# Kernel tuning notes

Hardware: AMD Instinct MI355X
Metric: run time of the kernel (lower is better)

## Reference

```python
import jax, jax.numpy as jnp
import numpy as np

R_MAX = 10.0
NUM_BESSEL = 8
POLY_P = 5
EMB = 64
MLP_DIM = 256
NUM_LAYERS = 3
IN_DIM = 10
OUT_DIM = 1
N_NODES = 256
N_EDGES = 1024
N_GRAPHS = 16
# gated TP output: 0e channel carries 64 scalars + 128 gates (one per gated 1o/2e irrep)
GATE_MUL = {0: 3 * EMB, 1: EMB, 2: EMB}
L0_PATHS = [(0, 0, 0), (0, 1, 1), (0, 2, 2)]  # in_irreps = 64x0e
LN_PATHS = [(0, 0, 0), (1, 1, 0), (2, 2, 0), (0, 1, 1), (1, 0, 1), (1, 2, 1), (2, 1, 1), (0, 2, 2), (2, 0, 2), (1, 1, 2), (2, 2, 2)]

def _npaths(paths):
    d = {0: 0, 1: 0, 2: 0}
    for _, _, l3 in paths:
        d[l3] += 1
    return d

L0_NP = _npaths(L0_PATHS)
LN_NP = _npaths(LN_PATHS)
L0_NUMEL = sum(EMB * GATE_MUL[l3] for _, _, l3 in L0_PATHS)   # 20480
LN_NUMEL = sum(EMB * GATE_MUL[l3] for _, _, l3 in LN_PATHS)   # 69632

# ---- real spherical harmonics, component normalization (||Y_l||^2 = 2l+1) ----
def _sh_np(v):
    x, y, z = v[:, 0], v[:, 1], v[:, 2]
    s15 = np.sqrt(15.0)
    return {0: np.ones((v.shape[0], 1)),
            1: np.sqrt(3.0) * np.stack([x, y, z], 1),
            2: np.stack([s15 * x * y, s15 * y * z, 0.5 * np.sqrt(5.0) * (3 * z * z - 1), s15 * x * z, 0.5 * s15 * (x * x - y * y)], 1)}

def _rot(axis, t):
    c, s = np.cos(t), np.sin(t)
    R = np.eye(3)
    i, j = [(1, 2), (2, 0), (0, 1)][axis]
    R[i, i] = c; R[j, j] = c; R[i, j] = -s; R[j, i] = s
    return R

_PTS = np.random.RandomState(0).randn(64, 3)
_PTS /= np.linalg.norm(_PTS, axis=1, keepdims=True)

def _D(l, R):
    # rep matrix D with Y(Rv) = D @ Y(v), fit by least squares over sample points
    A = _sh_np(_PTS)[l]
    B = _sh_np(_PTS @ R.T)[l]
    return np.linalg.lstsq(A, B, rcond=None)[0].T

def _gen(l, axis, eps=1e-4):
    return (_D(l, _rot(axis, eps)) - _D(l, _rot(axis, -eps))) / (2 * eps)

def _cg(l1, l2, l3):
    # Clebsch-Gordan tensor as null space of the infinitesimal equivariance constraint
    d1, d2, d3 = 2 * l1 + 1, 2 * l2 + 1, 2 * l3 + 1
    rows = []
    for a in range(3):
        J1, J2, J3 = _gen(l1, a), _gen(l2, a), _gen(l3, a)
        rows.append(np.kron(J1.T, np.eye(d2 * d3)) + np.kron(np.eye(d1), np.kron(J2.T, np.eye(d3))) - np.kron(np.eye(d1 * d2), J3))
    _, _, Vh = np.linalg.svd(np.vstack(rows))
    c = Vh[-1].reshape(d1, d2, d3)
    c = c / np.linalg.norm(c)
    c = c * np.sign(c.flat[int(np.argmax(np.abs(c)))])
    return c

CG = {p: jnp.asarray(_cg(*p), jnp.float32) for p in set(LN_PATHS)}

def _sh_jax(u):
    x, y, z = u[..., 0], u[..., 1], u[..., 2]
    s15 = 15.0 ** 0.5
    return {0: jnp.ones_like(x)[:, None],
            1: (3.0 ** 0.5) * jnp.stack([x, y, z], -1),
            2: jnp.stack([s15 * x * y, s15 * y * z, 0.5 * (5.0 ** 0.5) * (3 * z * z - 1), s15 * x * z, 0.5 * s15 * (x * x - y * y)], -1)}

def _radial(r):
    # Bessel radial basis * polynomial cutoff envelope (MACE-style RadialEmbeddingBlock)
    n = jnp.arange(1, NUM_BESSEL + 1, dtype=r.dtype)
    bessel = (2.0 / R_MAX) ** 0.5 * jnp.sin(n * jnp.pi * r[:, None] / R_MAX) / r[:, None]
    x = r / R_MAX
    p = POLY_P
    env = 1.0 - 0.5 * (p + 1) * (p + 2) * x ** p + p * (p + 2) * x ** (p + 1) - 0.5 * p * (p + 1) * x ** (p + 2)
    env = env * (x < 1.0)
    return bessel * env[:, None]

def _conv(h, sh, ef, recv, send, paths, n_per, w1, b1, w2, b2):
    # TensorProductConvLayer: MLP(edge_feats) -> TP weights, CG tensor product, scatter-sum, gate
    E = ef.shape[0]
    w = jax.nn.relu(ef @ w1 + b1) @ w2 + b2  # (E, weight_numel)
    msgs = {0: 0.0, 1: 0.0, 2: 0.0}
    off = 0
    for (l1, l2, l3) in paths:
        mv = GATE_MUL[l3]
        wp = w[:, off:off + EMB * mv].reshape(E, EMB, mv)
        off += EMB * mv
        tmp = jnp.einsum('eui,ej,ijk->euk', h[l1][send], sh[l2], CG[(l1, l2, l3)])
        alpha = float(1.0 / np.sqrt(EMB * n_per[l3]))  # fan-in path normalization
        msgs[l3] = msgs[l3] + alpha * jnp.einsum('euk,euv->evk', tmp, wp)
    agg = {l: jax.ops.segment_sum(msgs[l], recv, num_segments=N_NODES) for l in msgs}
    s = agg[0][..., 0]  # (N, 192): 64 scalars + 128 gates
    return {0: jax.nn.silu(s[:, :EMB])[:, :, None],
            1: agg[1] * jax.nn.sigmoid(s[:, EMB:2 * EMB])[:, :, None],
            2: agg[2] * jax.nn.sigmoid(s[:, 2 * EMB:])[:, :, None]}

def _forward(atoms, pos, edge_index, batch, emb, l0_fc1_w, l0_fc1_b, l0_fc2_w, l0_fc2_b, fcs1_w, fcs1_b, fcs2_w, fcs2_b, pred_w1, pred_b1, pred_w2, pred_b2):
    recv, send = edge_index[0], edge_index[1]
    vec = pos[recv] - pos[send]
    r = jnp.maximum(jnp.linalg.norm(vec, axis=-1), 1e-6)
    sh = _sh_jax(vec / r[:, None])
    ef = _radial(r)
    h = {0: emb[atoms][:, :, None]}  # (N, 64, 1) scalar features
    h_new = _conv(h, sh, ef, recv, send, L0_PATHS, L0_NP, l0_fc1_w, l0_fc1_b, l0_fc2_w, l0_fc2_b)
    h_new[0] = h_new[0] + h[0]  # residual; F.pad means only scalar block overlaps
    h = h_new
    for i in range(NUM_LAYERS - 1):
        h_new = _conv(h, sh, ef, recv, send, LN_PATHS, LN_NP, fcs1_w[i], fcs1_b[i], fcs2_w[i], fcs2_b[i])
        h = {l: h_new[l] + h[l] for l in h_new}
    pooled = jax.ops.segment_sum(h[0][..., 0], batch, num_segments=N_GRAPHS)  # out[:, :emb_dim]
    return jax.nn.relu(pooled @ pred_w1 + pred_b1) @ pred_w2 + pred_b2

def setup_inputs():
    key = jax.random.key(0)
    ks = jax.random.split(key, 12)
    def lin(k, fi, fo):
        return jax.random.normal(k, (fi, fo), jnp.float32) * float(1.0 / np.sqrt(fi))
    return dict(
        atoms=jax.random.randint(ks[0], (N_NODES,), 0, IN_DIM),
        pos=jax.random.normal(ks[1], (N_NODES, 3), jnp.float32) * 2.0,
        edge_index=jax.random.randint(ks[2], (2, N_EDGES), 0, N_NODES),
        batch=jnp.sort(jax.random.randint(ks[3], (N_NODES,), 0, N_GRAPHS)),
        emb=jax.random.normal(ks[4], (IN_DIM, EMB), jnp.float32),
        l0_fc1_w=lin(ks[5], NUM_BESSEL, MLP_DIM), l0_fc1_b=jnp.zeros((MLP_DIM,), jnp.float32),
        l0_fc2_w=lin(ks[6], MLP_DIM, L0_NUMEL), l0_fc2_b=jnp.zeros((L0_NUMEL,), jnp.float32),
        fcs1_w=jax.random.normal(ks[7], (NUM_LAYERS - 1, NUM_BESSEL, MLP_DIM), jnp.float32) * float(1.0 / np.sqrt(NUM_BESSEL)),
        fcs1_b=jnp.zeros((NUM_LAYERS - 1, MLP_DIM), jnp.float32),
        fcs2_w=jax.random.normal(ks[8], (NUM_LAYERS - 1, MLP_DIM, LN_NUMEL), jnp.float32) * float(1.0 / np.sqrt(MLP_DIM)),
        fcs2_b=jnp.zeros((NUM_LAYERS - 1, LN_NUMEL), jnp.float32),
        pred_w1=lin(ks[9], EMB, EMB), pred_b1=jnp.zeros((EMB,), jnp.float32),
        pred_w2=lin(ks[10], EMB, OUT_DIM), pred_b2=jnp.zeros((OUT_DIM,), jnp.float32),
    )

def reference(atoms, pos, edge_index, batch, emb, l0_fc1_w, l0_fc1_b, l0_fc2_w, l0_fc2_b, fcs1_w, fcs1_b, fcs2_w, fcs2_b, pred_w1, pred_b1, pred_w2, pred_b2):
    return _forward(atoms, pos, edge_index, batch, emb, l0_fc1_w, l0_fc1_b, l0_fc2_w, l0_fc2_b, fcs1_w, fcs1_b, fcs2_w, fcs2_b, pred_w1, pred_b1, pred_w2, pred_b2)
```

## Files before the change

### kernel.cpp

```cpp
#include <hip/hip_runtime.h>
#include <hip/hip_bf16.h>
#include <math.h>

#define NE 1024
#define NN 256
#define NG 16
#define EMB 64
#define KD 256
#define BK 64
#define NUMEL_L0 20480
#define NUMEL_LN 69632
#define MSGW 704
#define MAXE 256

typedef __attribute__((ext_vector_type(8))) __bf16 bf16x8;
typedef __attribute__((ext_vector_type(4))) float f32x4;
typedef __attribute__((ext_vector_type(4))) unsigned int u32x4;

__device__ __align__(16) float g_sh[NE * 8];
__device__ __align__(16) float g_ef[NE * 8];
__device__ __align__(16) unsigned short g_hidb[3][NE * KD];
__device__ __align__(16) unsigned short g_w2t0[(size_t)NUMEL_L0 * KD];
__device__ __align__(16) unsigned short g_w2t1[(size_t)NUMEL_LN * KD];
__device__ __align__(16) unsigned short g_w2t2[(size_t)NUMEL_LN * KD];
__device__ __align__(16) unsigned short g_wb[(size_t)NE * NUMEL_LN];
__device__ __align__(16) float g_msgs[NE * MSGW];
__device__ __align__(16) float g_h0[NN * EMB];
__device__ __align__(16) float g_h1[NN * EMB * 3];
__device__ __align__(16) float g_h2[NN * EMB * 5];
__device__ int g_elist[NN * MAXE];
__device__ int g_ecnt[NN];
__device__ float g_cg[363];

__device__ __forceinline__ unsigned short f2b(float x) {
    __hip_bfloat16 h = __float2bfloat16(x);
    return *(unsigned short*)&h;
}
__device__ __forceinline__ float b2f(unsigned short u) {
    __hip_bfloat16 h;
    *(unsigned short*)&h = u;
    return __bfloat162float(h);
}

__device__ __forceinline__ void gld16(const void* g, void* l) {
    __builtin_amdgcn_global_load_lds(
        (const __attribute__((address_space(1))) unsigned int*)g,
        (__attribute__((address_space(3))) unsigned int*)l, 16, 0, 0);
}

struct Path { int l1, l2, d1, d2, d3, mv, off, cgoff, tmpoff; };

__constant__ Path PLN[11] = {
    {0, 0, 1, 1, 1, 192, 0,     0,   0},
    {1, 1, 3, 3, 1, 192, 12288, 1,   64},
    {2, 2, 5, 5, 1, 192, 24576, 10,  128},
    {0, 1, 1, 3, 3, 64,  36864, 35,  192},
    {1, 0, 3, 1, 3, 64,  40960, 44,  384},
    {1, 2, 3, 5, 3, 64,  45056, 53,  576},
    {2, 1, 5, 3, 3, 64,  49152, 98,  768},
    {0, 2, 1, 5, 5, 64,  53248, 143, 960},
    {2, 0, 5, 1, 5, 64,  57344, 168, 1280},
    {1, 1, 3, 3, 5, 64,  61440, 193, 1600},
    {2, 2, 5, 5, 5, 64,  65536, 238, 1920},
};
__constant__ Path PL0[3] = {
    {0, 0, 1, 1, 1, 192, 0,     0,   0},
    {0, 1, 1, 3, 3, 64,  12288, 35,  64},
    {0, 2, 1, 5, 5, 64,  16384, 143, 256},
};

__device__ void init_cg_body() {
    for (int i = 0; i < 363; i++) g_cg[i] = 0.f;
    const float K3 = 0.57735026918962576f;
    const float K5 = 0.44721359549995794f;
    const float A  = 0.31622776601683794f;
    const float B  = 0.18257418583505536f;
    const float C2 = 0.36514837167011072f;
    const float P  = 0.23904572186687872f;
    const float Q  = 0.20701966780270626f;
    const float S  = 0.11952286093343936f;
    g_cg[0] = 1.f;
    for (int i = 0; i < 3; i++) g_cg[1 + i * 3 + i] = K3;
    for (int i = 0; i < 5; i++) g_cg[10 + i * 5 + i] = K5;
    for (int i = 0; i < 3; i++) g_cg[35 + i * 3 + i] = K3;
    for (int i = 0; i < 3; i++) g_cg[44 + i * 3 + i] = K3;
    g_cg[53 + 1]  = A;  g_cg[53 + 15] = A;  g_cg[53 + 20] = A;
    g_cg[53 + 34] = A;  g_cg[53 + 11] = A;  g_cg[53 + 39] = A;
    g_cg[53 + 6]  = -B; g_cg[53 + 22] = -B; g_cg[53 + 38] = C2;
    g_cg[53 + 12] = A;  g_cg[53 + 28] = -A;
    g_cg[98 + 1]  = A;  g_cg[98 + 3]  = A;  g_cg[98 + 14] = A;
    g_cg[98 + 16] = A;  g_cg[98 + 29] = A;  g_cg[98 + 33] = A;
    g_cg[98 + 18] = -B; g_cg[98 + 22] = -B; g_cg[98 + 26] = C2;
    g_cg[98 + 36] = A;  g_cg[98 + 40] = -A;
    for (int i = 0; i < 5; i++) g_cg[143 + i * 5 + i] = K5;
    for (int i = 0; i < 5; i++) g_cg[168 + i * 5 + i] = K5;
    g_cg[193 + 5]  = A;  g_cg[193 + 15] = A;  g_cg[193 + 26] = A;
    g_cg[193 + 36] = A;  g_cg[193 + 13] = A;  g_cg[193 + 33] = A;
    g_cg[193 + 2]  = -B; g_cg[193 + 22] = -B; g_cg[193 + 42] = C2;
    g_cg[193 + 4]  = A;  g_cg[193 + 24] = -A;
    g_cg[238 + 2]   = P;  g_cg[238 + 10]  = P;  g_cg[238 + 50]  = P;
    g_cg[238 + 8]   = -Q; g_cg[238 + 16]  = -Q; g_cg[238 + 28]  = -Q;
    g_cg[238 + 40]  = -Q; g_cg[238 + 76]  = -Q; g_cg[238 + 80]  = -Q;
    g_cg[238 + 32]  = -S; g_cg[238 + 36]  = -S; g_cg[238 + 56]  = -S;
    g_cg[238 + 34]  = Q;  g_cg[238 + 46]  = Q;  g_cg[238 + 106] = Q;
    g_cg[238 + 62]  = -P;
    g_cg[238 + 74]  = P;  g_cg[238 + 114] = P;  g_cg[238 + 122] = P;
    g_cg[238 + 68]  = -S; g_cg[238 + 88]  = -S; g_cg[238 + 92]  = -S;
    g_cg[238 + 94]  = -Q; g_cg[238 + 98]  = -Q; g_cg[238 + 118] = -Q;
}

__global__ __launch_bounds__(256) void k_setup(const int* ei, const float* pos,
                                               const int* atoms, const float* emb,
                                               const float* l0w2, const float* f2w) {
    int bid = blockIdx.x, tid = threadIdx.x;
    if (bid == 0) {
        if (tid == 0) init_cg_body();
        return;
    }
    if (bid <= 4) {
        int e = (bid - 1) * 256 + tid;
        int recv = ei[e], send = ei[NE + e];
        float vx = pos[recv * 3 + 0] - pos[send * 3 + 0];
        float vy = pos[recv * 3 + 1] - pos[send * 3 + 1];
        float vz = pos[recv * 3 + 2] - pos[send * 3 + 2];
        float rn = sqrtf(vx * vx + vy * vy + vz * vz);
        float r = fmaxf(rn, 1e-6f);
        float x = vx / r, y = vy / r, z = vz / r;
        const float S3 = 1.7320508075688772f;
        const float S15 = 3.8729833462074170f;
        const float S5H = 1.1180339887498949f;
        const float S15H = 1.9364916731037085f;
        g_sh[e * 8 + 0] = S3 * x;
        g_sh[e * 8 + 1] = S3 * y;
        g_sh[e * 8 + 2] = S3 * z;
        g_sh[e * 8 + 3] = S15 * x * y;
        g_sh[e * 8 + 4] = S15 * y * z;
        g_sh[e * 8 + 5] = S5H * (3.f * z * z - 1.f);
        g_sh[e * 8 + 6] = S15 * x * z;
        g_sh[e * 8 + 7] = S15H * (x * x - y * y);
        float xr = r * 0.1f;
        float env = 0.f;
        if (xr < 1.f) {
            float x5 = xr * xr * xr * xr * xr;
            env = 1.f - 21.f * x5 + 35.f * x5 * xr - 15.f * x5 * xr * xr;
        }
        const float SB = 0.44721359549995794f;
        const float PI = 3.14159265358979323846f;
        for (int nb = 1; nb <= 8; nb++) {
            g_ef[e * 8 + nb - 1] = SB * sinf((float)nb * PI * r * 0.1f) / r * env;
        }
        return;
    }
    if (bid <= 68) {
        int idx = (bid - 5) * 256 + tid;
        int n = idx / EMB, u = idx % EMB;
        g_h0[idx] = emb[atoms[n] * EMB + u];
        for (int k = 0; k < 3; k++) g_h1[idx * 3 + k] = 0.f;
        for (int k = 0; k < 5; k++) g_h2[idx * 5 + k] = 0.f;
        return;
    }
    if (bid <= 324) {
        int n = bid - 69;
        int lane = tid & 63, w = tid >> 6;
        __shared__ int wsum[4];
        int mask = 0;
#pragma unroll
        for (int i = 0; i < 4; i++) {
            if (ei[tid * 4 + i] == n) mask |= 1 << i;
        }
        int nm = __popc(mask);
        int incl = nm;
#pragma unroll
        for (int off = 1; off < 64; off <<= 1) {
            int v = __shfl_up(incl, off);
            if (lane >= off) incl += v;
        }
        if (lane == 63) wsum[w] = incl;
        __syncthreads();
        int wbase = 0;
        for (int i = 0; i < w; i++) wbase += wsum[i];
        int base = wbase + incl - nm;
#pragma unroll
        for (int i = 0; i < 4; i++) {
            if (mask & (1 << i)) g_elist[n * MAXE + base++] = tid * 4 + i;
        }
        if (tid == 255) g_ecnt[n] = wbase + incl;
        return;
    }
    {
        __shared__ float t[32][33];
        int wbid = bid - 325;
        int lbid, numel;
        const float* w2;
        unsigned short* dst;
        if (wbid < 5120)       { lbid = wbid;         numel = NUMEL_L0; w2 = l0w2; dst = g_w2t0; }
        else if (wbid < 22528) { lbid = wbid - 5120;  numel = NUMEL_LN; w2 = f2w;  dst = g_w2t1; }
        else                   { lbid = wbid - 22528; numel = NUMEL_LN;
                                 w2 = f2w + (size_t)KD * NUMEL_LN; dst = g_w2t2; }
        int n0 = (lbid >> 3) * 32, k0 = (lbid & 7) * 32;
        int tx = tid & 31, ty = tid >> 5;
#pragma unroll
        for (int i = 0; i < 4; i++) {
            int kl = ty * 4 + i;
            t[kl][tx] = w2[(size_t)(k0 + kl) * numel + n0 + tx];
        }
        __syncthreads();
#pragma unroll
        for (int i = 0; i < 4; i++) {
            int nl = ty * 4 + i;
            dst[(size_t)(n0 + nl) * KD + k0 + tx] = f2b(t[tx][nl]);
        }
    }
}

__global__ __launch_bounds__(256) void k_hid_all(const float* l0w1, const float* l0b1,
                                                 const float* f1w, const float* f1b) {
    int r = blockIdx.x;
    int layer = r >> 10, e = r & 1023;
    const float* w1 = layer == 0 ? l0w1 : f1w + (size_t)(layer - 1) * 8 * KD;
    const float* b1 = layer == 0 ? l0b1 : f1b + (size_t)(layer - 1) * KD;
    int m = threadIdx.x;
    float acc = b1[m];
    for (int nb = 0; nb < 8; nb++) acc += g_ef[e * 8 + nb] * w1[nb * KD + m];
    g_hidb[layer][e * KD + m] = f2b(fmaxf(acc, 0.f));
}

__global__ __launch_bounds__(256) void k_gemm_mfma(const float* b2, int numel, int layer) {
    __shared__ unsigned short S[16384];
    int tid = threadIdx.x;
    int lane = tid & 63, wid = tid >> 6;
    int wm = wid >> 1, wn = wid & 1;
    int id = blockIdx.x;
    int xcd = id & 7;
    int q = id >> 3;
    int mb = q & 7;
    int ytile = q >> 3;
    int nt = xcd + 8 * ytile;
    int m0 = mb * 128, n0 = nt * 128;
    int fr = lane & 15;
    int ko = (lane >> 4) * 8;

    const unsigned short* w2t = layer == 0 ? g_w2t0 : (layer == 1 ? g_w2t1 : g_w2t2);
    const char* gA = (const char*)g_hidb[layer];
    const char* gB = (const char*)w2t;
    f32x4 acc[4][4] = {};

    for (int kst = 0; kst < 4; kst++) {
#pragma unroll
        for (int i = 0; i < 4; i++) {
            int L = wid * 4096 + i * 1024 + lane * 16;
            int row = L >> 7, p = L & 127;
            int sp = p ^ ((row & 7) << 4);
            gld16(gA + ((size_t)(m0 + row) * KD + kst * BK) * 2 + sp, (char*)S + L);
        }
#pragma unroll
        for (int i = 0; i < 4; i++) {
            int L = wid * 4096 + i * 1024 + lane * 16;
            int row = L >> 7, p = L & 127;
            int sp = p ^ ((row & 7) << 4);
            gld16(gB + ((size_t)(n0 + row) * KD + kst * BK) * 2 + sp, (char*)S + 16384 + L);
        }
        __syncthreads();
#pragma unroll
        for (int ks = 0; ks < 2; ks++) {
            int klb = ks * 64 + ko * 2;
            bf16x8 af[4], bf_[4];
#pragma unroll
            for (int f = 0; f < 4; f++) {
                int ra = wm * 64 + f * 16 + fr;
                af[f] = *(bf16x8*)((char*)S + ra * 128 + (klb ^ ((ra & 7) << 4)));
                int rb = wn * 64 + f * 16 + fr;
                bf_[f] = *(bf16x8*)((char*)S + 16384 + rb * 128 + (klb ^ ((rb & 7) << 4)));
            }
#pragma unroll
            for (int i = 0; i < 4; i++)
#pragma unroll
                for (int j = 0; j < 4; j++)
                    acc[i][j] = __builtin_amdgcn_mfma_f32_16x16x32_bf16(af[i], bf_[j], acc[i][j], 0, 0, 0);
        }
        __syncthreads();
    }

#pragma unroll
    for (int j = 0; j < 4; j++) {
        int colL = wn * 64 + j * 16 + fr;
        float bb = b2[n0 + colL];
#pragma unroll
        for (int i = 0; i < 4; i++) {
#pragma unroll
            for (int r = 0; r < 4; r++) {
                int rowL = wm * 64 + i * 16 + (lane >> 4) * 4 + r;
                *(unsigned short*)((char*)S + rowL * 256 + ((colL * 2) ^ ((rowL & 7) << 4))) =
                    f2b(acc[i][j][r] + bb);
            }
        }
    }
    __syncthreads();
    for (int c = tid; c < 2048; c += 256) {
        int row = c >> 4, p16 = (c & 15) * 16;
        u32x4 v = *(u32x4*)((char*)S + row * 256 + (p16 ^ ((row & 7) << 4)));
        *(u32x4*)((char*)(g_wb + (size_t)(m0 + row) * numel + n0) + p16) = v;
    }
}

__global__ __launch_bounds__(256) void k_contract(const int* ei, int layer) {
    int e = blockIdx.x;
    int grp = blockIdx.y;
    int tid = threadIdx.x;
    __shared__ float tmp[1280];
    int layer0 = (layer == 0) ? 1 : 0;
    int numel = layer0 ? NUMEL_L0 : NUMEL_LN;
    const Path* PT = layer0 ? PL0 : PLN;
    int npaths = layer0 ? 3 : 11;
    int pstart = layer0 ? grp : (grp == 0 ? 0 : (grp == 1 ? 3 : 7));
    int pend   = layer0 ? grp + 1 : (grp == 0 ? 3 : (grp == 1 ? 7 : 11));
    int tbase = PT[pstart].tmpoff;
    int tend  = (pend < npaths) ? PT[pend].tmpoff : (layer0 ? 576 : 2240);
    int ttot = tend - tbase;
    const unsigned short* wrow = g_wb + (size_t)e * numel;
    int send = ei[NE + e];

    for (int t = tid; t < ttot; t += 256) {
        int tt = t + tbase;
        int p = pend - 1;
        while (tt < PT[p].tmpoff) p--;
        Path pp = PT[p];
        int rem = tt - pp.tmpoff;
        int u = rem / pp.d3, k = rem % pp.d3;
        float acc = 0.f;
        for (int i = 0; i < pp.d1; i++) {
            float hv = (pp.l1 == 0) ? g_h0[send * EMB + u]
                     : (pp.l1 == 1) ? g_h1[(send * EMB + u) * 3 + i]
                                    : g_h2[(send * EMB + u) * 5 + i];
            for (int j = 0; j < pp.d2; j++) {
                float sv = (pp.l2 == 0) ? 1.f
                         : (pp.l2 == 1 ? g_sh[e * 8 + j] : g_sh[e * 8 + 3 + j]);
                acc += hv * sv * g_cg[pp.cgoff + (i * pp.d2 + j) * pp.d3 + k];
            }
        }
        tmp[t] = acc;
    }
    __syncthreads();

    float alpha0 = layer0 ? 0.125f : 0.07216878364870323f;
    float alpha12 = layer0 ? 0.125f : 0.0625f;
    int v3 = tid / 3, k3 = tid - v3 * 3;
    int v5a = tid / 5, k5a = tid - v5a * 5;
    int p5b = 256 + tid;
    int v5b = p5b / 5, k5b = p5b - v5b * 5;
    float a0 = 0.f, a1 = 0.f;

    for (int p = pstart; p < pend; p++) {
        Path pp = PT[p];
        int to = pp.tmpoff - tbase;
        const unsigned short* wp = wrow + pp.off;
        if (pp.d3 == 1) {
            if (tid < 192) {
#pragma unroll 16
                for (int u = 0; u < 64; u++)
                    a0 += tmp[to + u] * b2f(wp[u * 192 + tid]);
            }
        } else if (pp.d3 == 3) {
            if (tid < 192) {
#pragma unroll 16
                for (int u = 0; u < 64; u++)
                    a0 += tmp[to + u * 3 + k3] * b2f(wp[u * 64 + v3]);
            }
        } else {
#pragma unroll 16
            for (int u = 0; u < 64; u++)
                a0 += tmp[to + u * 5 + k5a] * b2f(wp[u * 64 + v5a]);
            if (tid < 64) {
#pragma unroll 16
                for (int u = 0; u < 64; u++)
                    a1 += tmp[to + u * 5 + k5b] * b2f(wp[u * 64 + v5b]);
            }
        }
    }
    if (grp == 0) {
        if (tid < 192) g_msgs[e * MSGW + tid] = alpha0 * a0;
    } else if (grp == 1) {
        if (tid < 192) g_msgs[e * MSGW + 192 + tid] = alpha12 * a0;
    } else {
        g_msgs[e * MSGW + 384 + tid] = alpha12 * a0;
        if (tid < 64) g_msgs[e * MSGW + 640 + tid] = alpha12 * a1;
    }
}

__global__ __launch_bounds__(256) void k_agggate() {
    int n = blockIdx.x, tid = threadIdx.x;
    __shared__ float agg[MSGW];
    int cnt = g_ecnt[n];
    for (int d = tid; d < MSGW; d += 256) {
        float a = 0.f;
        for (int idx = 0; idx < cnt; idx++) {
            int e = g_elist[n * MAXE + idx];
            a += g_msgs[e * MSGW + d];
        }
        agg[d] = a;
    }
    __syncthreads();
    if (tid < EMB) {
        int u = tid;
        float s0 = agg[u], s1 = agg[64 + u], s2 = agg[128 + u];
        float sg0 = 1.f / (1.f + expf(-s0));
        float g0 = s0 * sg0;
        float sg1 = 1.f / (1.f + expf(-s1));
        float sg2 = 1.f / (1.f + expf(-s2));
        g_h0[n * EMB + u] += g0;
        for (int k = 0; k < 3; k++) g_h1[(n * EMB + u) * 3 + k] += agg[192 + u * 3 + k] * sg1;
        for (int k = 0; k < 5; k++) g_h2[(n * EMB + u) * 5 + k] += agg[384 + u * 5 + k] * sg2;
    }
}

__global__ __launch_bounds__(1024) void k_poolhead(const int* batch, const float* w1,
                                                   const float* b1, const float* w2,
                                                   const float* b2, float* out) {
    __shared__ float pl[NG * EMB];
    int g = threadIdx.x >> 6, u = threadIdx.x & 63;
    float a = 0.f;
    for (int n = 0; n < NN; n++)
        if (batch[n] == g) a += g_h0[n * EMB + u];
    pl[g * EMB + u] = a;
    __syncthreads();
    float t = b1[u];
    for (int uu = 0; uu < EMB; uu++) t += pl[g * EMB + uu] * w1[uu * EMB + u];
    t = fmaxf(t, 0.f);
    float contrib = t * w2[u];
    for (int off = 32; off > 0; off >>= 1) contrib += __shfl_down(contrib, off);
    if (u == 0) out[g] = contrib + b2[0];
}

extern "C" void kernel_launch(void* const* d_in, const int* in_sizes, int n_in,
                              void* d_out, int out_size, void* d_ws, size_t ws_size,
                              hipStream_t stream) {
    const int* atoms = (const int*)d_in[0];
    const float* pos = (const float*)d_in[1];
    const int* ei = (const int*)d_in[2];
    const int* batch = (const int*)d_in[3];
    const float* emb = (const float*)d_in[4];
    const float* l0w1 = (const float*)d_in[5];
    const float* l0b1 = (const float*)d_in[6];
    const float* l0w2 = (const float*)d_in[7];
    const float* l0b2 = (const float*)d_in[8];
    const float* f1w = (const float*)d_in[9];
    const float* f1b = (const float*)d_in[10];
    const float* f2w = (const float*)d_in[11];
    const float* f2b_ = (const float*)d_in[12];
    const float* pw1 = (const float*)d_in[13];
    const float* pb1 = (const float*)d_in[14];
    const float* pw2 = (const float*)d_in[15];
    const float* pb2 = (const float*)d_in[16];
    float* out = (float*)d_out;

    k_setup<<<dim3(40261), dim3(256), 0, stream>>>(ei, pos, atoms, emb, l0w2, f2w);
    k_hid_all<<<dim3(3072), dim3(256), 0, stream>>>(l0w1, l0b1, f1w, f1b);

    for (int layer = 0; layer < 3; layer++) {
        const float* b2 = layer == 0 ? l0b2 : f2b_ + (size_t)(layer - 1) * NUMEL_LN;
        int numel = layer == 0 ? NUMEL_L0 : NUMEL_LN;
        k_gemm_mfma<<<dim3((numel / 128) * (NE / 128)), dim3(256), 0, stream>>>(b2, numel, layer);
        k_contract<<<dim3(NE, 3), dim3(256), 0, stream>>>(ei, layer);
        k_agggate<<<dim3(NN), dim3(256), 0, stream>>>();
    }

    k_poolhead<<<dim3(1), dim3(1024), 0, stream>>>(batch, pw1, pb1, pw2, pb2, out);
}
```

Before: 421.3 us.

## Fuse radial MLP hidden layer into setup kernel and widen weight transpose tiles

Folds the first radial MLP layer into the setup kernel as extra blocks that recompute edge length, envelope and Bessel features inline, so the separate hidden-layer launch and its dependency on g_ef go away. The weight transpose-to-bf16 path moves from 32x32 tiles with scalar loads and stores to 64x64 tiles with float4 loads and 8-wide bf16 packed stores, which cuts the block count. The transpose blocks are also reordered. The cost is recomputing sinf per edge per thread and a larger shared tile.

```diff
diff --git a/kernel.cpp b/kernel.cpp
--- a/kernel.cpp
+++ b/kernel.cpp
@@ -16,6 +16,7 @@
 typedef __attribute__((ext_vector_type(8))) __bf16 bf16x8;
 typedef __attribute__((ext_vector_type(4))) float f32x4;
 typedef __attribute__((ext_vector_type(4))) unsigned int u32x4;
+typedef __attribute__((ext_vector_type(8))) unsigned short u16x8;
 
 __device__ __align__(16) float g_sh[NE * 8];
 __device__ __align__(16) float g_ef[NE * 8];
@@ -111,7 +112,9 @@
 
 __global__ __launch_bounds__(256) void k_setup(const int* ei, const float* pos,
                                                const int* atoms, const float* emb,
-                                               const float* l0w2, const float* f2w) {
+                                               const float* l0w2, const float* f2w,
+                                               const float* l0w1, const float* l0b1,
+                                               const float* f1w, const float* f1b) {
     int bid = blockIdx.x, tid = threadIdx.x;
     if (bid == 0) {
         if (tid == 0) init_cg_body();
@@ -187,42 +190,64 @@
         if (tid == 255) g_ecnt[n] = wbase + incl;
         return;
     }
+    if (bid <= 3396) {
+        int r_ = bid - 325;
+        int layer = r_ >> 10, e = r_ & 1023;
+        const float* w1 = layer == 0 ? l0w1 : f1w + (size_t)(layer - 1) * 8 * KD;
+        const float* b1 = layer == 0 ? l0b1 : f1b + (size_t)(layer - 1) * KD;
+        int m = tid;
+        int recv = ei[e], send = ei[NE + e];
+        float vx = pos[recv * 3 + 0] - pos[send * 3 + 0];
+        float vy = pos[recv * 3 + 1] - pos[send * 3 + 1];
+        float vz = pos[recv * 3 + 2] - pos[send * 3 + 2];
+        float rn = sqrtf(vx * vx + vy * vy + vz * vz);
+        float r = fmaxf(rn, 1e-6f);
+        float xr = r * 0.1f;
+        float env = 0.f;
+        if (xr < 1.f) {
+            float x5 = xr * xr * xr * xr * xr;
+            env = 1.f - 21.f * x5 + 35.f * x5 * xr - 15.f * x5 * xr * xr;
+        }
+        const float SB = 0.44721359549995794f;
+        const float PI = 3.14159265358979323846f;
+        float acc = b1[m];
+        for (int nb = 1; nb <= 8; nb++) {
+            float ef = SB * sinf((float)nb * PI * r * 0.1f) / r * env;
+            acc += ef * w1[(nb - 1) * KD + m];
+        }
+        g_hidb[layer][e * KD + m] = f2b(fmaxf(acc, 0.f));
+        return;
+    }
     {
-        __shared__ float t[32][33];
-        int wbid = bid - 325;
+        __shared__ float t[64][65];
+        int wbid = bid - 3397;
         int lbid, numel;
         const float* w2;
         unsigned short* dst;
-        if (wbid < 5120)       { lbid = wbid;         numel = NUMEL_L0; w2 = l0w2; dst = g_w2t0; }
-        else if (wbid < 22528) { lbid = wbid - 5120;  numel = NUMEL_LN; w2 = f2w;  dst = g_w2t1; }
-        else                   { lbid = wbid - 22528; numel = NUMEL_LN;
-                                 w2 = f2w + (size_t)KD * NUMEL_LN; dst = g_w2t2; }
-        int n0 = (lbid >> 3) * 32, k0 = (lbid & 7) * 32;
-        int tx = tid & 31, ty = tid >> 5;
-#pragma unroll
-        for (int i = 0; i < 4; i++) {
-            int kl = ty * 4 + i;
-            t[kl][tx] = w2[(size_t)(k0 + kl) * numel + n0 + tx];
+        if (wbid < 4352)      { lbid = wbid;        numel = NUMEL_LN; w2 = f2w + (size_t)KD * NUMEL_LN; dst = g_w2t2; }
+        else if (wbid < 8704) { lbid = wbid - 4352; numel = NUMEL_LN; w2 = f2w;  dst = g_w2t1; }
+        else                  { lbid = wbid - 8704; numel = NUMEL_L0; w2 = l0w2; dst = g_w2t0; }
+        int ntile = lbid >> 2, ktile = lbid & 3;
+        int n0 = ntile * 64, k0 = ktile * 64;
+        for (int c = tid; c < 1024; c += 256) {
+            int row = c >> 4, c4 = (c & 15) * 4;
+            f32x4 v = *(const f32x4*)&w2[(size_t)(k0 + row) * numel + n0 + c4];
+            t[row][c4 + 0] = v[0];
+            t[row][c4 + 1] = v[1];
+            t[row][c4 + 2] = v[2];
+            t[row][c4 + 3] = v[3];
         }
         __syncthreads();
 #pragma unroll
-        for (int i = 0; i < 4; i++) {
-            int nl = ty * 4 + i;
-            dst[(size_t)(n0 + nl) * KD + k0 + tx] = f2b(t[tx][nl]);
-        }
-    }
-}
-
-__global__ __launch_bounds__(256) void k_hid_all(const float* l0w1, const float* l0b1,
-                                                 const float* f1w, const float* f1b) {
-    int r = blockIdx.x;
-    int layer = r >> 10, e = r & 1023;
-    const float* w1 = layer == 0 ? l0w1 : f1w + (size_t)(layer - 1) * 8 * KD;
-    const float* b1 = layer == 0 ? l0b1 : f1b + (size_t)(layer - 1) * KD;
-    int m = threadIdx.x;
-    float acc = b1[m];
-    for (int nb = 0; nb < 8; nb++) acc += g_ef[e * 8 + nb] * w1[nb * KD + m];
-    g_hidb[layer][e * KD + m] = f2b(fmaxf(acc, 0.f));
+        for (int it = 0; it < 2; it++) {
+            int ch = tid + it * 256;
+            int n = ch >> 3, k8 = (ch & 7) * 8;
+            u16x8 pk;
+#pragma unroll
+            for (int i = 0; i < 8; i++) pk[i] = f2b(t[k8 + i][n]);
+            *(u16x8*)&dst[(size_t)(n0 + n) * KD + k0 + k8] = pk;
+        }
+    }
 }
 
 __global__ __launch_bounds__(256) void k_gemm_mfma(const float* b2, int numel, int layer) {
@@ -453,8 +478,8 @@
     const float* pb2 = (const float*)d_in[16];
     float* out = (float*)d_out;
 
-    k_setup<<<dim3(40261), dim3(256), 0, stream>>>(ei, pos, atoms, emb, l0w2, f2w);
-    k_hid_all<<<dim3(3072), dim3(256), 0, stream>>>(l0w1, l0b1, f1w, f1b);
+    k_setup<<<dim3(13381), dim3(256), 0, stream>>>(ei, pos, atoms, emb, l0w2, f2w,
+                                                   l0w1, l0b1, f1w, f1b);
 
     for (int layer = 0; layer < 3; layer++) {
         const float* b2 = layer == 0 ? l0b2 : f2b_ + (size_t)(layer - 1) * NUMEL_LN;
```

Result: slower. 433.4 us (+2.9%).

## Overlap next layer's weight GEMM with current layer's contraction in one launch

Applied to the files above, without the earlier changes.

Gives each layer its own per-edge weight buffer. The GEMM and contraction bodies become device functions, and a combined kernel runs layer L's contraction blocks alongside layer L+1's weight GEMM blocks. The next layer's GEMM does not depend on the current layer's node features, so the two can share the GPU, which removes serialization and a kernel launch per layer. The cost is extra global memory for the separate weight buffers, higher LDS use per block in the fused kernel (GEMM and contraction scratch together), and block-order dependence for the overlap.

```diff
diff --git a/kernel.cpp b/kernel.cpp
--- a/kernel.cpp
+++ b/kernel.cpp
@@ -23,7 +23,9 @@
 __device__ __align__(16) unsigned short g_w2t0[(size_t)NUMEL_L0 * KD];
 __device__ __align__(16) unsigned short g_w2t1[(size_t)NUMEL_LN * KD];
 __device__ __align__(16) unsigned short g_w2t2[(size_t)NUMEL_LN * KD];
-__device__ __align__(16) unsigned short g_wb[(size_t)NE * NUMEL_LN];
+__device__ __align__(16) unsigned short g_wb0[(size_t)NE * NUMEL_L0];
+__device__ __align__(16) unsigned short g_wb1[(size_t)NE * NUMEL_LN];
+__device__ __align__(16) unsigned short g_wb2[(size_t)NE * NUMEL_LN];
 __device__ __align__(16) float g_msgs[NE * MSGW];
 __device__ __align__(16) float g_h0[NN * EMB];
 __device__ __align__(16) float g_h1[NN * EMB * 3];
@@ -225,14 +227,13 @@
     g_hidb[layer][e * KD + m] = f2b(fmaxf(acc, 0.f));
 }
 
-__global__ __launch_bounds__(256) void k_gemm_mfma(const float* b2, int numel, int layer) {
-    __shared__ unsigned short S[16384];
+__device__ __forceinline__ void gemm_body(unsigned short* S, int lid, int layer,
+                                          const float* b2, int numel) {
     int tid = threadIdx.x;
     int lane = tid & 63, wid = tid >> 6;
     int wm = wid >> 1, wn = wid & 1;
-    int id = blockIdx.x;
-    int xcd = id & 7;
-    int q = id >> 3;
+    int xcd = lid & 7;
+    int q = lid >> 3;
     int mb = q & 7;
     int ytile = q >> 3;
     int nt = xcd + 8 * ytile;
@@ -241,6 +242,7 @@
     int ko = (lane >> 4) * 8;
 
     const unsigned short* w2t = layer == 0 ? g_w2t0 : (layer == 1 ? g_w2t1 : g_w2t2);
+    unsigned short* wb = layer == 0 ? g_wb0 : (layer == 1 ? g_wb1 : g_wb2);
     const char* gA = (const char*)g_hidb[layer];
     const char* gB = (const char*)w2t;
     f32x4 acc[4][4] = {};
@@ -299,17 +301,16 @@
     for (int c = tid; c < 2048; c += 256) {
         int row = c >> 4, p16 = (c & 15) * 16;
         u32x4 v = *(u32x4*)((char*)S + row * 256 + (p16 ^ ((row & 7) << 4)));
-        *(u32x4*)((char*)(g_wb + (size_t)(m0 + row) * numel + n0) + p16) = v;
-    }
-}
-
-__global__ __launch_bounds__(256) void k_contract(const int* ei, int layer) {
-    int e = blockIdx.x;
-    int grp = blockIdx.y;
+        *(u32x4*)((char*)(wb + (size_t)(m0 + row) * numel + n0) + p16) = v;
+    }
+}
+
+__device__ __forceinline__ void contract_body(float* tmp, const int* ei, int layer,
+                                              int e, int grp) {
     int tid = threadIdx.x;
-    __shared__ float tmp[1280];
     int layer0 = (layer == 0) ? 1 : 0;
     int numel = layer0 ? NUMEL_L0 : NUMEL_LN;
+    const unsigned short* wbase = layer == 0 ? g_wb0 : (layer == 1 ? g_wb1 : g_wb2);
     const Path* PT = layer0 ? PL0 : PLN;
     int npaths = layer0 ? 3 : 11;
     int pstart = layer0 ? grp : (grp == 0 ? 0 : (grp == 1 ? 3 : 7));
@@ -317,7 +318,7 @@
     int tbase = PT[pstart].tmpoff;
     int tend  = (pend < npaths) ? PT[pend].tmpoff : (layer0 ? 576 : 2240);
     int ttot = tend - tbase;
-    const unsigned short* wrow = g_wb + (size_t)e * numel;
+    const unsigned short* wrow = wbase + (size_t)e * numel;
     int send = ei[NE + e];
 
     for (int t = tid; t < ttot; t += 256) {
@@ -384,6 +385,28 @@
     } else {
         g_msgs[e * MSGW + 384 + tid] = alpha12 * a0;
         if (tid < 64) g_msgs[e * MSGW + 640 + tid] = alpha12 * a1;
+    }
+}
+
+__global__ __launch_bounds__(256) void k_gemm(const float* b2, int numel, int layer) {
+    __shared__ __align__(16) unsigned short S[16384];
+    gemm_body(S, blockIdx.x, layer, b2, numel);
+}
+
+__global__ __launch_bounds__(256) void k_contract(const int* ei, int layer) {
+    __shared__ __align__(16) float tmp[1280];
+    contract_body(tmp, ei, layer, blockIdx.x, blockIdx.y);
+}
+
+__global__ __launch_bounds__(256) void k_cx_gemm(const int* ei, int layer_c,
+                                                 const float* b2, int numel_g, int layer_g) {
+    __shared__ __align__(16) unsigned short S[16384];
+    __shared__ __align__(16) float tmp[1280];
+    int bid = blockIdx.x;
+    if (bid < 3072) {
+        contract_body(tmp, ei, layer_c, bid & 1023, bid >> 10);
+    } else {
+        gemm_body(S, bid - 3072, layer_g, b2, numel_g);
     }
 }
 
@@ -456,13 +479,15 @@
     k_setup<<<dim3(40261), dim3(256), 0, stream>>>(ei, pos, atoms, emb, l0w2, f2w);
     k_hid_all<<<dim3(3072), dim3(256), 0, stream>>>(l0w1, l0b1, f1w, f1b);
 
-    for (int layer = 0; layer < 3; layer++) {
-        const float* b2 = layer == 0 ? l0b2 : f2b_ + (size_t)(layer - 1) * NUMEL_LN;
-        int numel = layer == 0 ? NUMEL_L0 : NUMEL_LN;
-        k_gemm_mfma<<<dim3((numel / 128) * (NE / 128)), dim3(256), 0, stream>>>(b2, numel, layer);
-        k_contract<<<dim3(NE, 3), dim3(256), 0, stream>>>(ei, layer);
-        k_agggate<<<dim3(NN), dim3(256), 0, stream>>>();
-    }
+    k_gemm<<<dim3((NUMEL_L0 / 128) * (NE / 128)), dim3(256), 0, stream>>>(l0b2, NUMEL_L0, 0);
+    k_cx_gemm<<<dim3(3072 + (NUMEL_LN / 128) * (NE / 128)), dim3(256), 0, stream>>>(
+        ei, 0, f2b_, NUMEL_LN, 1);
+    k_agggate<<<dim3(NN), dim3(256), 0, stream>>>();
+    k_cx_gemm<<<dim3(3072 + (NUMEL_LN / 128) * (NE / 128)), dim3(256), 0, stream>>>(
+        ei, 1, f2b_ + NUMEL_LN, NUMEL_LN, 2);
+    k_agggate<<<dim3(NN), dim3(256), 0, stream>>>();
+    k_contract<<<dim3(NE, 3), dim3(256), 0, stream>>>(ei, 2);
+    k_agggate<<<dim3(NN), dim3(256), 0, stream>>>();
 
     k_poolhead<<<dim3(1), dim3(1024), 0, stream>>>(batch, pw1, pb1, pw2, pb2, out);
 }
```

Measured after the change: 478.5 us. 13.6% more time.

## Reorganize weight transpose into K-chunked bf16 layout with vectorized loads and stores

Applied to the files above, without the earlier changes.

The setup kernel's fc2 weight transpose now handles 64x256 tiles per block instead of 32x32. It reads fp32 with float4 loads, converts to bf16 in shared memory, and writes 16-byte packed stores. The transposed weights are stored as K-chunked [kt][n][64] slabs, so the GEMM B-tile loads become contiguous 128-byte rows per chunk. The block count drops sharply and the block order is changed. The shared tile has 264-element rows, which may cause LDS bank conflicts on the column reads.

```diff
diff --git a/kernel.cpp b/kernel.cpp
--- a/kernel.cpp
+++ b/kernel.cpp
@@ -16,6 +16,7 @@
 typedef __attribute__((ext_vector_type(8))) __bf16 bf16x8;
 typedef __attribute__((ext_vector_type(4))) float f32x4;
 typedef __attribute__((ext_vector_type(4))) unsigned int u32x4;
+typedef __attribute__((ext_vector_type(8))) unsigned short u16x8;
 
 __device__ __align__(16) float g_sh[NE * 8];
 __device__ __align__(16) float g_ef[NE * 8];
@@ -188,27 +189,32 @@
         return;
     }
     {
-        __shared__ float t[32][33];
+        __shared__ unsigned short t16[64][264];
         int wbid = bid - 325;
         int lbid, numel;
         const float* w2;
         unsigned short* dst;
-        if (wbid < 5120)       { lbid = wbid;         numel = NUMEL_L0; w2 = l0w2; dst = g_w2t0; }
-        else if (wbid < 22528) { lbid = wbid - 5120;  numel = NUMEL_LN; w2 = f2w;  dst = g_w2t1; }
-        else                   { lbid = wbid - 22528; numel = NUMEL_LN;
-                                 w2 = f2w + (size_t)KD * NUMEL_LN; dst = g_w2t2; }
-        int n0 = (lbid >> 3) * 32, k0 = (lbid & 7) * 32;
-        int tx = tid & 31, ty = tid >> 5;
-#pragma unroll
-        for (int i = 0; i < 4; i++) {
-            int kl = ty * 4 + i;
-            t[kl][tx] = w2[(size_t)(k0 + kl) * numel + n0 + tx];
+        if (wbid < 1088)      { lbid = wbid;        numel = NUMEL_LN; w2 = f2w + (size_t)KD * NUMEL_LN; dst = g_w2t2; }
+        else if (wbid < 2176) { lbid = wbid - 1088; numel = NUMEL_LN; w2 = f2w;  dst = g_w2t1; }
+        else                  { lbid = wbid - 2176; numel = NUMEL_L0; w2 = l0w2; dst = g_w2t0; }
+        int ntile = lbid >> 2, kt = lbid & 3;
+        int n0 = ntile * 256, k0 = kt * BK;
+        for (int c = tid; c < 4096; c += 256) {
+            int row = c >> 6, c4 = (c & 63) * 4;
+            f32x4 v = *(const f32x4*)&w2[(size_t)(k0 + row) * numel + n0 + c4];
+            t16[row][c4 + 0] = f2b(v[0]);
+            t16[row][c4 + 1] = f2b(v[1]);
+            t16[row][c4 + 2] = f2b(v[2]);
+            t16[row][c4 + 3] = f2b(v[3]);
         }
         __syncthreads();
-#pragma unroll
-        for (int i = 0; i < 4; i++) {
-            int nl = ty * 4 + i;
-            dst[(size_t)(n0 + nl) * KD + k0 + tx] = f2b(t[tx][nl]);
+        u16x8* dstp = (u16x8*)&dst[((size_t)kt * numel + n0 + tid) * BK];
+#pragma unroll
+        for (int i = 0; i < 8; i++) {
+            u16x8 pk;
+#pragma unroll
+            for (int j = 0; j < 8; j++) pk[j] = t16[i * 8 + j][tid];
+            dstp[i] = pk;
         }
     }
 }
@@ -258,7 +264,7 @@
             int L = wid * 4096 + i * 1024 + lane * 16;
             int row = L >> 7, p = L & 127;
             int sp = p ^ ((row & 7) << 4);
-            gld16(gB + ((size_t)(n0 + row) * KD + kst * BK) * 2 + sp, (char*)S + 16384 + L);
+            gld16(gB + ((size_t)kst * numel + n0 + row) * 128 + sp, (char*)S + 16384 + L);
         }
         __syncthreads();
 #pragma unroll
@@ -453,7 +459,7 @@
     const float* pb2 = (const float*)d_in[16];
     float* out = (float*)d_out;
 
-    k_setup<<<dim3(40261), dim3(256), 0, stream>>>(ei, pos, atoms, emb, l0w2, f2w);
+    k_setup<<<dim3(2821), dim3(256), 0, stream>>>(ei, pos, atoms, emb, l0w2, f2w);
     k_hid_all<<<dim3(3072), dim3(256), 0, stream>>>(l0w1, l0b1, f1w, f1b);
 
     for (int layer = 0; layer < 3; layer++) {
```

After: 442.0 us. 1.05x slower.
